# Kernel tuning notes

Measured on AMD Instinct MI355X. Metric: run time of the kernel, lower is better.

## Reference

```python
import jax, jax.numpy as jnp
import numpy as np

PRIMES = [250007, 250013, 250027, 250031, 250037, 250043, 250049, 250051]
OFFSETS = np.concatenate([[0], np.cumsum(PRIMES)[:-1]]).astype(np.int64)  # [8]
TOTAL_ROWS = int(np.sum(PRIMES))
D_HEAD = 128          # embedding_dim_per_head
E_DIM = 8 * D_HEAD    # total_embedding_dim = 1024
H_DIM = 2560          # hidden_dim
KSIZE = 4             # causal depthwise conv kernel
EPS = 1e-6


def rmsnorm(x, g):
    # torch.nn.RMSNorm: x / sqrt(mean(x^2) + eps) * weight
    return x * jax.lax.rsqrt(jnp.mean(x * x, axis=-1, keepdims=True) + EPS) * g


def setup_inputs() -> dict:
    key = jax.random.key(0)
    ks = jax.random.split(key, 10)
    B, L = 4, 4096
    return {
        "hidden_states": jax.random.normal(ks[0], (B, L, H_DIM), jnp.float32),
        "engram_hash_indices": jax.random.randint(ks[1], (B, L, 8), 0, 250007, jnp.int64),
        "emb_table": jax.random.normal(ks[2], (TOTAL_ROWS, D_HEAD), jnp.float32) * 0.02,
        "w_v": jax.random.normal(ks[3], (H_DIM, E_DIM), jnp.float32) * 0.02,
        "w_k": jax.random.normal(ks[4], (H_DIM, E_DIM), jnp.float32) * 0.02,
        "g_h": jnp.ones((H_DIM,), jnp.float32),
        "g_k": jnp.ones((H_DIM,), jnp.float32),
        "g_v": jnp.ones((H_DIM,), jnp.float32),
        # paper zero-inits the conv; use small random weights so the conv path is exercised
        "conv_w": jax.random.normal(ks[5], (H_DIM, KSIZE), jnp.float32) * 0.02,
        "conv_b": jax.random.normal(ks[6], (H_DIM,), jnp.float32) * 0.02,
    }


def reference(hidden_states, engram_hash_indices, emb_table, w_v, w_k, g_h, g_k, g_v, conv_w, conv_b):
    B, L, H = hidden_states.shape
    # multi-head hash embedding retrieval
    idx = engram_hash_indices + jnp.asarray(OFFSETS)            # [B,L,8]
    e_t = emb_table[idx].reshape(B, L, E_DIM)                    # gather + concat heads
    # value / key projections (Linear, no bias)
    v_t = jnp.einsum('ble,he->blh', e_t, w_v)                    # [B,L,H]
    k_t = jnp.einsum('ble,he->blh', e_t, w_k)
    # context-aware gating
    h_n = rmsnorm(hidden_states, g_h)
    k_n = rmsnorm(k_t, g_k)
    dot = jnp.sum(h_n * k_n, axis=-1) / jnp.sqrt(jnp.float32(H))  # [B,L]
    stable = jnp.sqrt(jnp.maximum(jnp.abs(dot), 1e-6)) * jnp.sign(dot)
    alpha = jax.nn.sigmoid(stable)                               # [B,L]
    v_tilde = alpha[..., None] * v_t                             # [B,L,H]
    v_n = rmsnorm(v_tilde, g_v)
    # causal depthwise conv1d (left pad K-1) + SiLU
    x_pad = jnp.pad(v_n, ((0, 0), (KSIZE - 1, 0), (0, 0)))       # [B,L+3,H]
    conv = sum(conv_w[:, j] * x_pad[:, j:j + L, :] for j in range(KSIZE)) + conv_b
    y = jax.nn.silu(conv) + v_tilde
    return hidden_states + y
```

## Files before the change

kernel.cpp:

```cpp
#include <hip/hip_runtime.h>
#include <cstddef>
#include <cstdint>

typedef __bf16 bf16;
typedef __bf16 bf16x4 __attribute__((ext_vector_type(4)));
typedef __bf16 bf16x8 __attribute__((ext_vector_type(8)));
typedef float f32x4 __attribute__((ext_vector_type(4)));

#define AS1C(p) ((const __attribute__((address_space(1))) void*)(p))
#define AS3(p)  ((__attribute__((address_space(3))) void*)(p))

#define MROWS 16384
#define HDIM 2560
#define EDIM 1024
#define LSEQ 4096

static __device__ const int kHeadOff[8] = {0, 250007, 500020, 750047,
                                           1000078, 1250115, 1500158, 1750207};

__global__ __launch_bounds__(256) void k_gather(const int* __restrict__ hidx,
                                                const float* __restrict__ emb,
                                                bf16* __restrict__ E) {
  const int m = blockIdx.x;
  const int t = threadIdx.x;
  const int head = t >> 5;
  const int e4 = (t & 31) * 4;
  const int rid = hidx[m * 8 + head] + kHeadOff[head];
  const float4 v = *(const float4*)(emb + (size_t)rid * 128 + e4);
  bf16x4 o;
  o[0] = (bf16)v.x; o[1] = (bf16)v.y; o[2] = (bf16)v.z; o[3] = (bf16)v.w;
  *(bf16x4*)(E + (size_t)m * EDIM + head * 128 + e4) = o;
}

__global__ __launch_bounds__(256) void k_cvt(const float* __restrict__ src,
                                             bf16* __restrict__ dst, int n) {
  int i = (blockIdx.x * 256 + threadIdx.x) * 8;
  if (i + 8 > n) return;
  float4 a = *(const float4*)(src + i);
  float4 b = *(const float4*)(src + i + 4);
  bf16x8 o;
  o[0] = (bf16)a.x; o[1] = (bf16)a.y; o[2] = (bf16)a.z; o[3] = (bf16)a.w;
  o[4] = (bf16)b.x; o[5] = (bf16)b.y; o[6] = (bf16)b.z; o[7] = (bf16)b.w;
  *(bf16x8*)(dst + i) = o;
}

__device__ __forceinline__ float red16(float v) {
  v += __shfl_xor(v, 1);
  v += __shfl_xor(v, 2);
  v += __shfl_xor(v, 4);
  v += __shfl_xor(v, 8);
  return v;
}


#define LDSB 24576

__global__ __launch_bounds__(512, 4) void k_gemm(const bf16* __restrict__ A,
                                                 const bf16* __restrict__ Wv,
                                                 const bf16* __restrict__ Wk,
                                                 const float* __restrict__ hidden,
                                                 const float* __restrict__ g_h,
                                                 const float* __restrict__ g_k,
                                                 bf16* __restrict__ Vt,
                                                 float* __restrict__ S) {
  __shared__ __attribute__((aligned(16))) char ldsc[2 * LDSB];
  const int tid = threadIdx.x;
  const int wid = tid >> 6, lane = tid & 63;
  const int wm = wid >> 1, wn = wid & 1;
  const int r16 = lane & 15, khalf = lane >> 4;

  const int w = blockIdx.x;
  const int xcd = w & 7;
  const int r_ = w >> 3;
  const int gx = r_ >> 3;
  const int y = xcd * 8 + (r_ & 7);
  const int m0 = y * 256;
  const bool isV = (gx < 20);
  const int n0 = (isV ? gx : gx - 20) * 128;
  const bf16* Wp = isV ? Wv : Wk;

  const int sw = ((r16 >> 1) & 3) << 4;
  const int c0 = (khalf * 16) ^ sw;
  const int aRd = (wm * 64 + r16) * 64 + c0;
  const int bRd = 16384 + (wn * 64 + r16) * 64 + c0;

  const int srow = tid >> 2;
  const int scol = (((tid & 3) ^ ((tid >> 3) & 3))) * 8;
  const bf16* pA0 = A + (size_t)(m0 + srow) * EDIM + scol;
  const bf16* pA1 = pA0 + (size_t)128 * EDIM;
  const bf16* pB = Wp + (size_t)(n0 + srow) * EDIM + scol;
  const int ldsW = wid * 1024;

  f32x4 acc[4][4] = {};

#define STAGE(BUFO, KT) do {                                                   \
    __builtin_amdgcn_global_load_lds(AS1C(pA0 + (KT) * 32),                    \
        AS3(ldsc + (BUFO) + ldsW), 16, 0, 0);                                  \
    __builtin_amdgcn_global_load_lds(AS1C(pA1 + (KT) * 32),                    \
        AS3(ldsc + (BUFO) + 8192 + ldsW), 16, 0, 0);                           \
    __builtin_amdgcn_global_load_lds(AS1C(pB + (KT) * 32),                     \
        AS3(ldsc + (BUFO) + 16384 + ldsW), 16, 0, 0);                          \
    __builtin_amdgcn_sched_barrier(0);                                         \
  } while (0)

#define PHASE_CORE(BUFO) do {                                                  \
    bf16x8 aF[4], bF[4];                                                       \
    _Pragma("unroll") for (int mi = 0; mi < 4; ++mi)                           \
      aF[mi] = *(const bf16x8*)(ldsc + (BUFO) + aRd + mi * 1024);              \
    _Pragma("unroll") for (int nj = 0; nj < 4; ++nj)                           \
      bF[nj] = *(const bf16x8*)(ldsc + (BUFO) + bRd + nj * 1024);              \
    asm volatile("s_waitcnt lgkmcnt(0)" ::: "memory");                         \
    __builtin_amdgcn_sched_barrier(0);                                         \
    __builtin_amdgcn_s_setprio(1);                                             \
    _Pragma("unroll") for (int mi = 0; mi < 4; ++mi)                           \
      _Pragma("unroll") for (int nj = 0; nj < 4; ++nj)                         \
        acc[mi][nj] = __builtin_amdgcn_mfma_f32_16x16x32_bf16(                 \
            aF[mi], bF[nj], acc[mi][nj], 0, 0, 0);                             \
    __builtin_amdgcn_s_setprio(0);                                             \
    __builtin_amdgcn_s_barrier();                                              \
  } while (0)

#define VMCNT3() asm volatile("s_waitcnt vmcnt(3)" ::: "memory")
#define VMCNT0() asm volatile("s_waitcnt vmcnt(0)" ::: "memory")

  STAGE(0, 0);
  STAGE(LDSB, 1);

  for (int p = 0; p < 30; p += 2) {
    VMCNT3();
    __builtin_amdgcn_s_barrier();
    PHASE_CORE(0);
    STAGE(0, p + 2);
    VMCNT3();
    __builtin_amdgcn_s_barrier();
    PHASE_CORE(LDSB);
    STAGE(LDSB, p + 3);
  }
  VMCNT3();
  __builtin_amdgcn_s_barrier();
  PHASE_CORE(0);
  VMCNT0();
  __builtin_amdgcn_s_barrier();
  PHASE_CORE(LDSB);

  float* P = (float*)ldsc;
  if (isV) {
#pragma unroll
    for (int mi = 0; mi < 4; ++mi) {
#pragma unroll
      for (int nj = 0; nj < 4; ++nj) {
        const int col = n0 + wn * 64 + nj * 16 + r16;
#pragma unroll
        for (int r = 0; r < 4; ++r) {
          const int row = m0 + wm * 64 + mi * 16 + khalf * 4 + r;
          Vt[(size_t)row * HDIM + col] = (bf16)acc[mi][nj][r];
        }
      }
#pragma unroll
      for (int r = 0; r < 4; ++r) {
        float p = 0.f;
#pragma unroll
        for (int nj = 0; nj < 4; ++nj) p += acc[mi][nj][r] * acc[mi][nj][r];
        p = red16(p);
        if (r16 == 0) {
          const int rl = wm * 64 + mi * 16 + khalf * 4 + r;
          P[wn * 256 + rl] = p;
        }
      }
    }
    __syncthreads();
    if (tid < 256) {
      const float s = P[tid] + P[256 + tid];
      atomicAdd(&S[(size_t)(m0 + tid) * 4 + 3], s);
    }
  } else {
    float ghk[4];
#pragma unroll
    for (int nj = 0; nj < 4; ++nj) {
      const int col = n0 + wn * 64 + nj * 16 + r16;
      ghk[nj] = g_h[col] * g_k[col];
    }
#pragma unroll
    for (int mi = 0; mi < 4; ++mi) {
#pragma unroll
      for (int r = 0; r < 4; ++r) {
        const int row = m0 + wm * 64 + mi * 16 + khalf * 4 + r;
        float p1 = 0.f, p2 = 0.f, p3 = 0.f;
#pragma unroll
        for (int nj = 0; nj < 4; ++nj) {
          const int col = n0 + wn * 64 + nj * 16 + r16;
          const float k = acc[mi][nj][r];
          const float h = hidden[(size_t)row * HDIM + col];
          p1 += h * h;
          p2 += h * ghk[nj] * k;
          p3 += k * k;
        }
        p1 = red16(p1); p2 = red16(p2); p3 = red16(p3);
        if (r16 == 0) {
          const int rl = wm * 64 + mi * 16 + khalf * 4 + r;
          float* Pr = P + (wn * 256 + rl) * 3;
          Pr[0] = p1; Pr[1] = p2; Pr[2] = p3;
        }
      }
    }
    __syncthreads();
    for (int j = tid; j < 768; j += 512) {
      const int rl = j / 3, c = j % 3;
      const float s = P[j] + P[768 + j];
      atomicAdd(&S[(size_t)(m0 + rl) * 4 + c], s);
    }
  }
#undef STAGE
#undef PHASE_CORE
#undef VMCNT3
#undef VMCNT0
}

__global__ __launch_bounds__(256) void k_scal(const float* __restrict__ S,
                                              float* __restrict__ AB) {
  const int m = blockIdx.x * 256 + threadIdx.x;
  const float s1 = S[(size_t)m * 4 + 0];
  const float s2 = S[(size_t)m * 4 + 1];
  const float s3 = S[(size_t)m * 4 + 2];
  const float s4 = S[(size_t)m * 4 + 3];
  const float inv_h = rsqrtf(s1 * (1.f / HDIM) + 1e-6f);
  const float inv_k = rsqrtf(s3 * (1.f / HDIM) + 1e-6f);
  const float dot = s2 * inv_h * inv_k * 0.019764235f;
  float st = sqrtf(fmaxf(fabsf(dot), 1e-6f));
  st = (dot < 0.f) ? -st : st;
  if (dot == 0.f) st = 0.f;
  const float alpha = 1.f / (1.f + __expf(-st));
  const float inv_v = rsqrtf(alpha * alpha * s4 * (1.f / HDIM) + 1e-6f);
  AB[(size_t)m * 2 + 0] = alpha;
  AB[(size_t)m * 2 + 1] = alpha * inv_v;
}

__global__ __launch_bounds__(320) void k_fuse(const float* __restrict__ hidden,
                                              const bf16* __restrict__ Vt,
                                              const float* __restrict__ AB,
                                              const float* __restrict__ g_v,
                                              const float* __restrict__ conv_w,
                                              const float* __restrict__ conv_b,
                                              float* __restrict__ out) {
  const int mbase = blockIdx.x * 8;
  const int l0 = mbase & (LSEQ - 1);
  const int t = threadIdx.x;
  const int h0 = t * 8;

  float gv[8], cb[8];
  *(float4*)&gv[0] = *(const float4*)(g_v + h0);
  *(float4*)&gv[4] = *(const float4*)(g_v + h0 + 4);
  *(float4*)&cb[0] = *(const float4*)(conv_b + h0);
  *(float4*)&cb[4] = *(const float4*)(conv_b + h0 + 4);
  float4 cw[8];
#pragma unroll
  for (int i = 0; i < 8; ++i)
    cw[i] = *(const float4*)(conv_w + (size_t)(h0 + i) * 4);

  float win[4][8];
#pragma unroll
  for (int jj = 0; jj < 4; ++jj)
#pragma unroll
    for (int i = 0; i < 8; ++i) win[jj][i] = 0.f;

#pragma unroll
  for (int j = 0; j < 11; ++j) {
    const int lj = l0 - 3 + j;
    const int m = mbase - 3 + j;
    float vtl[8];
    if (lj >= 0) {
      const float alpha = AB[(size_t)m * 2 + 0];
      const float av = AB[(size_t)m * 2 + 1];
      const bf16x8 v = *(const bf16x8*)(Vt + (size_t)m * HDIM + h0);
#pragma unroll
      for (int i = 0; i < 8; ++i) {
        const float vt = (float)v[i];
        vtl[i] = alpha * vt;
        win[j & 3][i] = av * vt * gv[i];
      }
    } else {
#pragma unroll
      for (int i = 0; i < 8; ++i) { win[j & 3][i] = 0.f; vtl[i] = 0.f; }
    }
    if (j >= 3) {
      const int R = mbase + j - 3;
      const size_t base = (size_t)R * HDIM + h0;
      float hx[8];
      *(float4*)&hx[0] = *(const float4*)(hidden + base);
      *(float4*)&hx[4] = *(const float4*)(hidden + base + 4);
      float o[8];
#pragma unroll
      for (int i = 0; i < 8; ++i) {
        float c = cb[i];
        c += ((const float*)&cw[i])[0] * win[(j - 3) & 3][i];
        c += ((const float*)&cw[i])[1] * win[(j - 2) & 3][i];
        c += ((const float*)&cw[i])[2] * win[(j - 1) & 3][i];
        c += ((const float*)&cw[i])[3] * win[j & 3][i];
        const float y = c / (1.f + __expf(-c));
        o[i] = hx[i] + y + vtl[i];
      }
      *(float4*)(out + base) = *(float4*)&o[0];
      *(float4*)(out + base + 4) = *(float4*)&o[4];
    }
  }
}

extern "C" void kernel_launch(void* const* d_in, const int* in_sizes, int n_in,
                              void* d_out, int out_size, void* d_ws,
                              size_t ws_size, hipStream_t stream) {
  const float* hidden = (const float*)d_in[0];
  const int* hashidx = (const int*)d_in[1];
  const float* emb = (const float*)d_in[2];
  const float* w_v = (const float*)d_in[3];
  const float* w_k = (const float*)d_in[4];
  const float* g_h = (const float*)d_in[5];
  const float* g_k = (const float*)d_in[6];
  const float* g_v = (const float*)d_in[7];
  const float* conv_w = (const float*)d_in[8];
  const float* conv_b = (const float*)d_in[9];
  float* out = (float*)d_out;

  char* w = (char*)d_ws;
  bf16* e16 = (bf16*)w;  w += (size_t)MROWS * EDIM * 2;
  bf16* wv16 = (bf16*)w; w += (size_t)HDIM * EDIM * 2;
  bf16* wk16 = (bf16*)w; w += (size_t)HDIM * EDIM * 2;
  bf16* vt16 = (bf16*)w; w += (size_t)MROWS * HDIM * 2;
  float* S = (float*)w;  w += (size_t)MROWS * 4 * 4;
  float* AB = (float*)w; w += (size_t)MROWS * 2 * 4;

  hipMemsetAsync(S, 0, (size_t)MROWS * 4 * 4, stream);
  k_gather<<<MROWS, 256, 0, stream>>>(hashidx, emb, e16);
  k_cvt<<<(HDIM * EDIM) / 2048, 256, 0, stream>>>(w_v, wv16, HDIM * EDIM);
  k_cvt<<<(HDIM * EDIM) / 2048, 256, 0, stream>>>(w_k, wk16, HDIM * EDIM);
  k_gemm<<<dim3(2560), 512, 0, stream>>>(e16, wv16, wk16, hidden, g_h, g_k,
                                         vt16, S);
  k_scal<<<MROWS / 256, 256, 0, stream>>>(S, AB);
  k_fuse<<<MROWS / 8, 320, 0, stream>>>(hidden, vt16, AB, g_v, conv_w, conv_b,
                                        out);
}
```

Baseline: 328.8 us.

## Merge weight conversions, widen gather vectors, and relax GEMM LDS wait placement

The two fp32-to-bf16 weight conversion launches are merged into a single kernel that picks its source by block index, which removes one launch. The gather kernel now handles two rows per block and loads eight floats per thread for 16-byte stores. In the GEMM inner phase, the LDS wait and scheduling barrier that sat before the MFMAs are removed and the wait is moved after them, and the MFMA loop order is swapped. This lets the compiler place per-fragment waits, at the risk of relying on its own waitcnt insertion.

```diff
diff --git a/kernel.cpp b/kernel.cpp
--- a/kernel.cpp
+++ b/kernel.cpp
@@ -21,26 +21,34 @@
 __global__ __launch_bounds__(256) void k_gather(const int* __restrict__ hidx,
                                                 const float* __restrict__ emb,
                                                 bf16* __restrict__ E) {
-  const int m = blockIdx.x;
   const int t = threadIdx.x;
-  const int head = t >> 5;
-  const int e4 = (t & 31) * 4;
+  const int m = blockIdx.x * 2 + (t >> 7);
+  const int tt = t & 127;
+  const int head = tt >> 4;
+  const int e8 = (tt & 15) * 8;
   const int rid = hidx[m * 8 + head] + kHeadOff[head];
-  const float4 v = *(const float4*)(emb + (size_t)rid * 128 + e4);
-  bf16x4 o;
-  o[0] = (bf16)v.x; o[1] = (bf16)v.y; o[2] = (bf16)v.z; o[3] = (bf16)v.w;
-  *(bf16x4*)(E + (size_t)m * EDIM + head * 128 + e4) = o;
-}
-
-__global__ __launch_bounds__(256) void k_cvt(const float* __restrict__ src,
-                                             bf16* __restrict__ dst, int n) {
-  int i = (blockIdx.x * 256 + threadIdx.x) * 8;
-  if (i + 8 > n) return;
+  const float4 v0 = *(const float4*)(emb + (size_t)rid * 128 + e8);
+  const float4 v1 = *(const float4*)(emb + (size_t)rid * 128 + e8 + 4);
+  bf16x8 o;
+  o[0] = (bf16)v0.x; o[1] = (bf16)v0.y; o[2] = (bf16)v0.z; o[3] = (bf16)v0.w;
+  o[4] = (bf16)v1.x; o[5] = (bf16)v1.y; o[6] = (bf16)v1.z; o[7] = (bf16)v1.w;
+  *(bf16x8*)(E + (size_t)m * EDIM + head * 128 + e8) = o;
+}
+
+__global__ __launch_bounds__(256) void k_cvt2(const float* __restrict__ s0,
+                                              bf16* __restrict__ d0,
+                                              const float* __restrict__ s1,
+                                              bf16* __restrict__ d1) {
+  int b = blockIdx.x;
+  const float* src = s0;
+  bf16* dst = d0;
+  if (b >= 1280) { b -= 1280; src = s1; dst = d1; }
+  const int i = (b * 256 + threadIdx.x) * 8;
   float4 a = *(const float4*)(src + i);
-  float4 b = *(const float4*)(src + i + 4);
+  float4 c = *(const float4*)(src + i + 4);
   bf16x8 o;
   o[0] = (bf16)a.x; o[1] = (bf16)a.y; o[2] = (bf16)a.z; o[3] = (bf16)a.w;
-  o[4] = (bf16)b.x; o[5] = (bf16)b.y; o[6] = (bf16)b.z; o[7] = (bf16)b.w;
+  o[4] = (bf16)c.x; o[5] = (bf16)c.y; o[6] = (bf16)c.z; o[7] = (bf16)c.w;
   *(bf16x8*)(dst + i) = o;
 }
 
@@ -109,38 +117,42 @@
       aF[mi] = *(const bf16x8*)(ldsc + (BUFO) + aRd + mi * 1024);              \
     _Pragma("unroll") for (int nj = 0; nj < 4; ++nj)                           \
       bF[nj] = *(const bf16x8*)(ldsc + (BUFO) + bRd + nj * 1024);              \
-    asm volatile("s_waitcnt lgkmcnt(0)" ::: "memory");                         \
-    __builtin_amdgcn_sched_barrier(0);                                         \
     __builtin_amdgcn_s_setprio(1);                                             \
-    _Pragma("unroll") for (int mi = 0; mi < 4; ++mi)                           \
-      _Pragma("unroll") for (int nj = 0; nj < 4; ++nj)                         \
+    _Pragma("unroll") for (int nj = 0; nj < 4; ++nj)                           \
+      _Pragma("unroll") for (int mi = 0; mi < 4; ++mi)                         \
         acc[mi][nj] = __builtin_amdgcn_mfma_f32_16x16x32_bf16(                 \
             aF[mi], bF[nj], acc[mi][nj], 0, 0, 0);                             \
     __builtin_amdgcn_s_setprio(0);                                             \
+    asm volatile("s_waitcnt lgkmcnt(0)" ::: "memory");                         \
     __builtin_amdgcn_s_barrier();                                              \
   } while (0)
 
-#define VMCNT3() asm volatile("s_waitcnt vmcnt(3)" ::: "memory")
-#define VMCNT0() asm volatile("s_waitcnt vmcnt(0)" ::: "memory")
+#define BEGIN_PHASE3() do {                                                    \
+    asm volatile("s_waitcnt vmcnt(3)" ::: "memory");                           \
+    __builtin_amdgcn_s_barrier();                                              \
+    asm volatile("" ::: "memory");                                             \
+  } while (0)
+
+#define BEGIN_PHASE0() do {                                                    \
+    asm volatile("s_waitcnt vmcnt(0)" ::: "memory");                           \
+    __builtin_amdgcn_s_barrier();                                              \
+    asm volatile("" ::: "memory");                                             \
+  } while (0)
 
   STAGE(0, 0);
   STAGE(LDSB, 1);
 
   for (int p = 0; p < 30; p += 2) {
-    VMCNT3();
-    __builtin_amdgcn_s_barrier();
+    BEGIN_PHASE3();
     PHASE_CORE(0);
     STAGE(0, p + 2);
-    VMCNT3();
-    __builtin_amdgcn_s_barrier();
+    BEGIN_PHASE3();
     PHASE_CORE(LDSB);
     STAGE(LDSB, p + 3);
   }
-  VMCNT3();
-  __builtin_amdgcn_s_barrier();
+  BEGIN_PHASE3();
   PHASE_CORE(0);
-  VMCNT0();
-  __builtin_amdgcn_s_barrier();
+  BEGIN_PHASE0();
   PHASE_CORE(LDSB);
 
   float* P = (float*)ldsc;
@@ -212,8 +224,8 @@
   }
 #undef STAGE
 #undef PHASE_CORE
-#undef VMCNT3
-#undef VMCNT0
+#undef BEGIN_PHASE3
+#undef BEGIN_PHASE0
 }
 
 __global__ __launch_bounds__(256) void k_scal(const float* __restrict__ S,
@@ -329,9 +341,8 @@
   float* AB = (float*)w; w += (size_t)MROWS * 2 * 4;
 
   hipMemsetAsync(S, 0, (size_t)MROWS * 4 * 4, stream);
-  k_gather<<<MROWS, 256, 0, stream>>>(hashidx, emb, e16);
-  k_cvt<<<(HDIM * EDIM) / 2048, 256, 0, stream>>>(w_v, wv16, HDIM * EDIM);
-  k_cvt<<<(HDIM * EDIM) / 2048, 256, 0, stream>>>(w_k, wk16, HDIM * EDIM);
+  k_gather<<<MROWS / 2, 256, 0, stream>>>(hashidx, emb, e16);
+  k_cvt2<<<2560, 256, 0, stream>>>(w_v, wv16, w_k, wk16);
   k_gemm<<<dim3(2560), 512, 0, stream>>>(e16, wv16, wk16, hidden, g_h, g_k,
                                          vt16, S);
   k_scal<<<MROWS / 256, 256, 0, stream>>>(S, AB);
```

New measurement: 325.4 us. Within noise of the previous version (-1.0%).
